# Performance work log

Measured on AMD Instinct MI355X. Metric: run time of the kernel, lower is better.

Reference implementation:

```python
import jax, jax.numpy as jnp
import numpy as np

# Synthetic taxonomy matching BuildDictionaries/Build_H_Matrix structure
N_O, N_F, N_G, N_S = 25, 150, 1200, 4800
PIQUETS = [0, N_O, N_O + N_F, N_O + N_F + N_G, N_O + N_F + N_G + N_S]  # [0,25,175,1375,6175]
C_TOTAL = PIQUETS[-1]
WEIGHTS = [0.25, 0.25, 0.15, 0.1]
E = float(np.e)
BATCH = 4096


def _build_H():
    H = np.zeros((C_TOTAL, C_TOTAL), dtype=np.float32)
    fam = np.arange(N_F)
    H[fam % N_O, PIQUETS[1] + fam] = 1.0              # order -> family
    gen = np.arange(N_G)
    H[PIQUETS[1] + gen % N_F, PIQUETS[2] + gen] = 1.0  # family -> genus
    sp = np.arange(N_S)
    H[PIQUETS[2] + sp % N_G, PIQUETS[3] + sp] = 1.0    # genus -> species
    return H


def setup_inputs() -> dict:
    key = jax.random.key(0)
    k1, k2 = jax.random.split(key)
    H_np = _build_H()
    # parent[j] = i such that H[i, j] == 1 (same as the get_grandparents row scan)
    parent_np = np.argmax(H_np, axis=0).astype(np.int64)
    y_pred = jax.random.normal(k1, (BATCH, C_TOTAL), dtype=jnp.float32)
    y_true = jax.random.randint(k2, (BATCH,), 0, N_S, dtype=jnp.int64)
    return {
        "y_pred": y_pred,
        "y_true": y_true,
        "H": jnp.asarray(H_np),
        "parent": jnp.asarray(parent_np),
    }


def _ce(logits, labels):
    # nn.CrossEntropyLoss with mean reduction
    logp = jax.nn.log_softmax(logits, axis=-1)
    return -jnp.mean(jnp.take_along_axis(logp, labels[:, None], axis=1))


def reference(y_pred, y_true, H, parent):
    nb_levels = 4
    # Per-level logit slices: y_pred[:, piquets[k]:piquets[k+1]]
    lp = [y_pred[:, PIQUETS[k]:PIQUETS[k + 1]] for k in range(nb_levels)]

    # Ancestor chain (vectorized get_grandparents): global ids per level
    g3 = y_true + PIQUETS[3]           # global species id (y_true += piquets[-2])
    g2 = parent[g3]                    # genus
    g1 = parent[g2]                    # family
    g0 = parent[g1]                    # order
    lt = [g0 - PIQUETS[0], g1 - PIQUETS[1], g2 - PIQUETS[2], g3 - PIQUETS[3]]

    # Faithful quirk: argmax indices are LOCAL to each level's slice,
    # and H is indexed with those local indices (as in the original code).
    argm = [jnp.argmax(x, axis=-1) for x in lp]

    s = _ce(lp[0], lt[0])
    loss = jnp.zeros((), dtype=y_pred.dtype)
    for k in range(1, nb_levels):
        h = H[argm[k - 1], argm[k]]                      # [B] gather
        pen = jnp.sum(jnp.where(h == 0, E, 0.0))         # sum_i (H==0)*e
        s = (s + pen + _ce(lp[k], lt[k])) * WEIGHTS[k]   # running sum *= weights[k]
        loss = loss + s
    return loss
```

## Files before the change

kernel.cpp:

```cpp
#include <hip/hip_runtime.h>
#include <math.h>

#define C_TOTAL 6175
#define BATCH 4096
#define NLEV 4

__device__ inline void am_merge(float& m, int& idx, float m2, int i2) {
    const bool take = (m2 > m) || (m2 == m && i2 < idx);
    idx = take ? i2 : idx;
    m   = fmaxf(m, m2);
}

__device__ inline void upd(float x, int i, float& m, float& s, int& ii) {
    s += __expf(x);
    ii = (x > m) ? i : ii;
    m  = fmaxf(m, x);
}

__device__ inline void butterfly(float& s, float& m, int& idx) {
    #pragma unroll
    for (int off = 1; off < 64; off <<= 1) {
        const float mm = __shfl_xor(m, off);
        const int   im = __shfl_xor(idx, off);
        const float sm = __shfl_xor(s, off);
        s += sm;
        am_merge(m, idx, mm, im);
    }
}

template <int W>
__device__ inline void process_span(const float* __restrict__ p,
                                    int lane, float& S, float& M, int& I) {
    if constexpr (W <= 64) {
        const float x = p[lane];
        const bool  a = (lane < W);
        float s = a ? __expf(x) : 0.f;
        float m = a ? x : -INFINITY;
        int idx = a ? lane : 0x7fffffff;
        butterfly(s, m, idx);
        S = s; M = m; I = idx;
        return;
    }

    float ms = -INFINITY, ss = 0.f;
    int   is_ = 0x7fffffff;

    int pe = (int)((4u - ((((uintptr_t)p) >> 2) & 3u)) & 3u);
    if (lane < pe) {
        const float x = p[lane];
        ss = __expf(x); ms = x; is_ = lane;
    }
    const int rem  = W - pe;
    const int nvec = rem >> 2;
    const int tail = rem & 3;
    const float4* vp = reinterpret_cast<const float4*>(p + pe);

    float m0 = -INFINITY, m1 = -INFINITY, m2 = -INFINITY, m3 = -INFINITY;
    float s0 = 0.f, s1 = 0.f, s2 = 0.f, s3 = 0.f;
    int   i0 = 0x1fffffff, i1 = 0x1fffffff, i2 = 0x1fffffff, i3 = 0x1fffffff;

    int i = lane;
    if constexpr (W >= 1024) {
        for (; i + 192 < nvec; i += 256) {
            const float4 a = vp[i];
            const float4 b = vp[i + 64];
            const float4 c = vp[i + 128];
            const float4 d = vp[i + 192];
            upd(a.x, i,       m0, s0, i0); upd(a.y, i,       m1, s1, i1);
            upd(a.z, i,       m2, s2, i2); upd(a.w, i,       m3, s3, i3);
            upd(b.x, i + 64,  m0, s0, i0); upd(b.y, i + 64,  m1, s1, i1);
            upd(b.z, i + 64,  m2, s2, i2); upd(b.w, i + 64,  m3, s3, i3);
            upd(c.x, i + 128, m0, s0, i0); upd(c.y, i + 128, m1, s1, i1);
            upd(c.z, i + 128, m2, s2, i2); upd(c.w, i + 128, m3, s3, i3);
            upd(d.x, i + 192, m0, s0, i0); upd(d.y, i + 192, m1, s1, i1);
            upd(d.z, i + 192, m2, s2, i2); upd(d.w, i + 192, m3, s3, i3);
        }
        for (; i + 64 < nvec; i += 128) {
            const float4 a = vp[i];
            const float4 b = vp[i + 64];
            upd(a.x, i, m0, s0, i0); upd(a.y, i, m1, s1, i1);
            upd(a.z, i, m2, s2, i2); upd(a.w, i, m3, s3, i3);
            upd(b.x, i + 64, m0, s0, i0); upd(b.y, i + 64, m1, s1, i1);
            upd(b.z, i + 64, m2, s2, i2); upd(b.w, i + 64, m3, s3, i3);
        }
    }
    for (; i < nvec; i += 64) {
        const float4 a = vp[i];
        upd(a.x, i, m0, s0, i0); upd(a.y, i, m1, s1, i1);
        upd(a.z, i, m2, s2, i2); upd(a.w, i, m3, s3, i3);
    }
    if (lane < tail) {
        const int c = pe + 4 * nvec + lane;
        const float x = p[c];
        ss += __expf(x);
        const bool take = (x > ms) || (x == ms && c < is_);
        is_ = take ? c : is_;
        ms  = fmaxf(ms, x);
    }

    float m = ms; int idx = is_;
    float s = ss + ((s0 + s1) + (s2 + s3));
    am_merge(m, idx, m0, pe + 4 * i0 + 0);
    am_merge(m, idx, m1, pe + 4 * i1 + 1);
    am_merge(m, idx, m2, pe + 4 * i2 + 2);
    am_merge(m, idx, m3, pe + 4 * i3 + 3);

    butterfly(s, m, idx);
    S = s; M = m; I = idx;
}

#define DO_SPAN(k, Wk)                                                      \
    {                                                                       \
        float S, M;                                                         \
        int I;                                                              \
        process_span<Wk>(rp + piq[k], lane, S, M, I);                       \
        ce[k]   = __logf(S) - rp[piq[k] + lab[k]];                          \
        argm[k] = I;                                                        \
    }

__global__ __launch_bounds__(256, 4) void taxa_row_kernel(
    const float* __restrict__ y_pred,
    const int*   __restrict__ y_true,
    const float* __restrict__ H,
    const int*   __restrict__ parent,
    float*       __restrict__ ws)
{
    constexpr int piq[5] = {0, 25, 175, 1375, 6175};
    const int lane = threadIdx.x & 63;
    const int wid  = threadIdx.x >> 6;
    const int row  = blockIdx.x * 4 + wid;
    const float* rp = y_pred + (long long)row * C_TOTAL;

    const int g3 = y_true[row] + 1375;
    const int g2 = parent[g3];
    const int g1 = parent[g2];
    const int g0 = parent[g1];
    int lab[NLEV];
    lab[0] = g0;
    lab[1] = g1 - 25;
    lab[2] = g2 - 175;
    lab[3] = g3 - 1375;

    float ce[NLEV];
    int   argm[NLEV];

    const int start = (blockIdx.x + wid) & 3;
    switch (start) {
        case 0: DO_SPAN(0, 25) DO_SPAN(1, 150) DO_SPAN(2, 1200) DO_SPAN(3, 4800) break;
        case 1: DO_SPAN(1, 150) DO_SPAN(2, 1200) DO_SPAN(3, 4800) DO_SPAN(0, 25) break;
        case 2: DO_SPAN(2, 1200) DO_SPAN(3, 4800) DO_SPAN(0, 25) DO_SPAN(1, 150) break;
        default: DO_SPAN(3, 4800) DO_SPAN(0, 25) DO_SPAN(1, 150) DO_SPAN(2, 1200) break;
    }

    if (lane == 0) {
        float h[3];
        #pragma unroll
        for (int k = 1; k < NLEV; ++k) {
            const float hv = H[(long long)argm[k - 1] * C_TOTAL + argm[k]];
            h[k - 1] = (hv == 0.f) ? 1.f : 0.f;
        }
        const float invB = 1.0f / 4096.0f;
        const float E    = 2.7182818284590452f;
        ws[row] = 0.29125f * ((ce[0] + ce[1]) * invB + E * h[0])
                + 0.165f  * (ce[2] * invB + E * h[1])
                + 0.10f   * (ce[3] * invB + E * h[2]);
    }
}

__global__ __launch_bounds__(256) void taxa_final_kernel(
    const float* __restrict__ ws, float* __restrict__ out)
{
    const int t = threadIdx.x;
    const float4* v = reinterpret_cast<const float4*>(ws);
    float a = 0.f;
    #pragma unroll
    for (int j = 0; j < 4; ++j) {
        const float4 x = v[t + 256 * j];
        a += (x.x + x.y) + (x.z + x.w);
    }
    #pragma unroll
    for (int off = 1; off < 64; off <<= 1) a += __shfl_xor(a, off);
    __shared__ float sm[4];
    if ((t & 63) == 0) sm[t >> 6] = a;
    __syncthreads();
    if (t == 0) out[0] = (sm[0] + sm[1]) + (sm[2] + sm[3]);
}

extern "C" void kernel_launch(void* const* d_in, const int* in_sizes, int n_in,
                              void* d_out, int out_size, void* d_ws, size_t ws_size,
                              hipStream_t stream) {
    const float* y_pred = (const float*)d_in[0];
    const int*   y_true = (const int*)d_in[1];
    const float* H      = (const float*)d_in[2];
    const int*   parent = (const int*)d_in[3];
    float* ws  = (float*)d_ws;
    float* out = (float*)d_out;

    taxa_row_kernel<<<dim3(BATCH / 4), dim3(256), 0, stream>>>(y_pred, y_true, H, parent, ws);
    taxa_final_kernel<<<dim3(1), dim3(256), 0, stream>>>(ws, out);
}
```

Baseline: 25.25 us.

## Process two rows per wavefront with interleaved loads for more memory-level parallelism

```diff
diff --git a/kernel.cpp b/kernel.cpp
--- a/kernel.cpp
+++ b/kernel.cpp
@@ -4,6 +4,7 @@
 #define C_TOTAL 6175
 #define BATCH 4096
 #define NLEV 4
+#define IBIG 0x1fffffff
 
 __device__ inline void am_merge(float& m, int& idx, float m2, int i2) {
     const bool take = (m2 > m) || (m2 == m && i2 < idx);
@@ -29,96 +30,126 @@
 }
 
 template <int W>
-__device__ inline void process_span(const float* __restrict__ p,
-                                    int lane, float& S, float& M, int& I) {
+__device__ inline void span2(const float* __restrict__ pA,
+                             const float* __restrict__ pB, int lane,
+                             float& SA, float& MA, int& IA,
+                             float& SB, float& MB, int& IB) {
     if constexpr (W <= 64) {
-        const float x = p[lane];
-        const bool  a = (lane < W);
-        float s = a ? __expf(x) : 0.f;
-        float m = a ? x : -INFINITY;
-        int idx = a ? lane : 0x7fffffff;
-        butterfly(s, m, idx);
-        S = s; M = m; I = idx;
+        const float xA = pA[lane];
+        const float xB = pB[lane];
+        const bool  a  = (lane < W);
+        float sA = a ? __expf(xA) : 0.f;
+        float mA = a ? xA : -INFINITY;
+        int   iA = a ? lane : 0x7fffffff;
+        float sB = a ? __expf(xB) : 0.f;
+        float mB = a ? xB : -INFINITY;
+        int   iB = a ? lane : 0x7fffffff;
+        butterfly(sA, mA, iA);
+        butterfly(sB, mB, iB);
+        SA = sA; MA = mA; IA = iA;
+        SB = sB; MB = mB; IB = iB;
         return;
     }
 
-    float ms = -INFINITY, ss = 0.f;
-    int   is_ = 0x7fffffff;
-
-    int pe = (int)((4u - ((((uintptr_t)p) >> 2) & 3u)) & 3u);
-    if (lane < pe) {
-        const float x = p[lane];
-        ss = __expf(x); ms = x; is_ = lane;
-    }
-    const int rem  = W - pe;
-    const int nvec = rem >> 2;
-    const int tail = rem & 3;
-    const float4* vp = reinterpret_cast<const float4*>(p + pe);
-
-    float m0 = -INFINITY, m1 = -INFINITY, m2 = -INFINITY, m3 = -INFINITY;
-    float s0 = 0.f, s1 = 0.f, s2 = 0.f, s3 = 0.f;
-    int   i0 = 0x1fffffff, i1 = 0x1fffffff, i2 = 0x1fffffff, i3 = 0x1fffffff;
-
+    const int peA = (int)((4u - ((((uintptr_t)pA) >> 2) & 3u)) & 3u);
+    const int peB = (int)((4u - ((((uintptr_t)pB) >> 2) & 3u)) & 3u);
+
+    float msA = -INFINITY, ssA = 0.f; int isA = 0x7fffffff;
+    float msB = -INFINITY, ssB = 0.f; int isB = 0x7fffffff;
+    if (lane < peA) { const float x = pA[lane]; ssA = __expf(x); msA = x; isA = lane; }
+    if (lane < peB) { const float x = pB[lane]; ssB = __expf(x); msB = x; isB = lane; }
+
+    const int nvA = (W - peA) >> 2, tlA = (W - peA) & 3;
+    const int nvB = (W - peB) >> 2, tlB = (W - peB) & 3;
+    const float4* vA = reinterpret_cast<const float4*>(pA + peA);
+    const float4* vB = reinterpret_cast<const float4*>(pB + peB);
+
+    float mA0=-INFINITY,mA1=-INFINITY,mA2=-INFINITY,mA3=-INFINITY;
+    float sA0=0.f,sA1=0.f,sA2=0.f,sA3=0.f;
+    int   iA0=IBIG,iA1=IBIG,iA2=IBIG,iA3=IBIG;
+    float mB0=-INFINITY,mB1=-INFINITY,mB2=-INFINITY,mB3=-INFINITY;
+    float sB0=0.f,sB1=0.f,sB2=0.f,sB3=0.f;
+    int   iB0=IBIG,iB1=IBIG,iB2=IBIG,iB3=IBIG;
+
+    const int nmin = nvA < nvB ? nvA : nvB;
     int i = lane;
     if constexpr (W >= 1024) {
-        for (; i + 192 < nvec; i += 256) {
-            const float4 a = vp[i];
-            const float4 b = vp[i + 64];
-            const float4 c = vp[i + 128];
-            const float4 d = vp[i + 192];
-            upd(a.x, i,       m0, s0, i0); upd(a.y, i,       m1, s1, i1);
-            upd(a.z, i,       m2, s2, i2); upd(a.w, i,       m3, s3, i3);
-            upd(b.x, i + 64,  m0, s0, i0); upd(b.y, i + 64,  m1, s1, i1);
-            upd(b.z, i + 64,  m2, s2, i2); upd(b.w, i + 64,  m3, s3, i3);
-            upd(c.x, i + 128, m0, s0, i0); upd(c.y, i + 128, m1, s1, i1);
-            upd(c.z, i + 128, m2, s2, i2); upd(c.w, i + 128, m3, s3, i3);
-            upd(d.x, i + 192, m0, s0, i0); upd(d.y, i + 192, m1, s1, i1);
-            upd(d.z, i + 192, m2, s2, i2); upd(d.w, i + 192, m3, s3, i3);
+        for (; i + 64 < nmin; i += 128) {
+            const float4 a0 = vA[i];
+            const float4 b0 = vB[i];
+            const float4 a1 = vA[i + 64];
+            const float4 b1 = vB[i + 64];
+            upd(a0.x, i,      mA0, sA0, iA0); upd(a0.y, i,      mA1, sA1, iA1);
+            upd(a0.z, i,      mA2, sA2, iA2); upd(a0.w, i,      mA3, sA3, iA3);
+            upd(b0.x, i,      mB0, sB0, iB0); upd(b0.y, i,      mB1, sB1, iB1);
+            upd(b0.z, i,      mB2, sB2, iB2); upd(b0.w, i,      mB3, sB3, iB3);
+            upd(a1.x, i + 64, mA0, sA0, iA0); upd(a1.y, i + 64, mA1, sA1, iA1);
+            upd(a1.z, i + 64, mA2, sA2, iA2); upd(a1.w, i + 64, mA3, sA3, iA3);
+            upd(b1.x, i + 64, mB0, sB0, iB0); upd(b1.y, i + 64, mB1, sB1, iB1);
+            upd(b1.z, i + 64, mB2, sB2, iB2); upd(b1.w, i + 64, mB3, sB3, iB3);
         }
-        for (; i + 64 < nvec; i += 128) {
-            const float4 a = vp[i];
-            const float4 b = vp[i + 64];
-            upd(a.x, i, m0, s0, i0); upd(a.y, i, m1, s1, i1);
-            upd(a.z, i, m2, s2, i2); upd(a.w, i, m3, s3, i3);
-            upd(b.x, i + 64, m0, s0, i0); upd(b.y, i + 64, m1, s1, i1);
-            upd(b.z, i + 64, m2, s2, i2); upd(b.w, i + 64, m3, s3, i3);
-        }
-    }
-    for (; i < nvec; i += 64) {
-        const float4 a = vp[i];
-        upd(a.x, i, m0, s0, i0); upd(a.y, i, m1, s1, i1);
-        upd(a.z, i, m2, s2, i2); upd(a.w, i, m3, s3, i3);
-    }
-    if (lane < tail) {
-        const int c = pe + 4 * nvec + lane;
-        const float x = p[c];
-        ss += __expf(x);
-        const bool take = (x > ms) || (x == ms && c < is_);
-        is_ = take ? c : is_;
-        ms  = fmaxf(ms, x);
-    }
-
-    float m = ms; int idx = is_;
-    float s = ss + ((s0 + s1) + (s2 + s3));
-    am_merge(m, idx, m0, pe + 4 * i0 + 0);
-    am_merge(m, idx, m1, pe + 4 * i1 + 1);
-    am_merge(m, idx, m2, pe + 4 * i2 + 2);
-    am_merge(m, idx, m3, pe + 4 * i3 + 3);
-
-    butterfly(s, m, idx);
-    S = s; M = m; I = idx;
-}
-
-#define DO_SPAN(k, Wk)                                                      \
+    }
+    int j = i;
+    for (; i < nvA; i += 64) {
+        const float4 a = vA[i];
+        upd(a.x, i, mA0, sA0, iA0); upd(a.y, i, mA1, sA1, iA1);
+        upd(a.z, i, mA2, sA2, iA2); upd(a.w, i, mA3, sA3, iA3);
+    }
+    for (; j < nvB; j += 64) {
+        const float4 b = vB[j];
+        upd(b.x, j, mB0, sB0, iB0); upd(b.y, j, mB1, sB1, iB1);
+        upd(b.z, j, mB2, sB2, iB2); upd(b.w, j, mB3, sB3, iB3);
+    }
+    if (lane < tlA) {
+        const int c = peA + 4 * nvA + lane;
+        const float x = pA[c];
+        ssA += __expf(x);
+        const bool take = (x > msA) || (x == msA && c < isA);
+        isA = take ? c : isA;
+        msA = fmaxf(msA, x);
+    }
+    if (lane < tlB) {
+        const int c = peB + 4 * nvB + lane;
+        const float x = pB[c];
+        ssB += __expf(x);
+        const bool take = (x > msB) || (x == msB && c < isB);
+        isB = take ? c : isB;
+        msB = fmaxf(msB, x);
+    }
+
+    {
+        float m = msA; int idx = isA;
+        float s = ssA + ((sA0 + sA1) + (sA2 + sA3));
+        am_merge(m, idx, mA0, peA + 4 * iA0 + 0);
+        am_merge(m, idx, mA1, peA + 4 * iA1 + 1);
+        am_merge(m, idx, mA2, peA + 4 * iA2 + 2);
+        am_merge(m, idx, mA3, peA + 4 * iA3 + 3);
+        butterfly(s, m, idx);
+        SA = s; MA = m; IA = idx;
+    }
+    {
+        float m = msB; int idx = isB;
+        float s = ssB + ((sB0 + sB1) + (sB2 + sB3));
+        am_merge(m, idx, mB0, peB + 4 * iB0 + 0);
+        am_merge(m, idx, mB1, peB + 4 * iB1 + 1);
+        am_merge(m, idx, mB2, peB + 4 * iB2 + 2);
+        am_merge(m, idx, mB3, peB + 4 * iB3 + 3);
+        butterfly(s, m, idx);
+        SB = s; MB = m; IB = idx;
+    }
+}
+
+#define DO_SPAN2(k, Wk)                                                     \
     {                                                                       \
-        float S, M;                                                         \
-        int I;                                                              \
-        process_span<Wk>(rp + piq[k], lane, S, M, I);                       \
-        ce[k]   = __logf(S) - rp[piq[k] + lab[k]];                          \
-        argm[k] = I;                                                        \
-    }
-
-__global__ __launch_bounds__(256, 4) void taxa_row_kernel(
+        float SA, MA, SB, MB;                                               \
+        int IA, IB;                                                         \
+        span2<Wk>(rpA + piq[k], rpB + piq[k], lane, SA, MA, IA, SB, MB, IB);\
+        ceA[k] = __logf(SA) - rpA[piq[k] + labA[k]];                        \
+        ceB[k] = __logf(SB) - rpB[piq[k] + labB[k]];                        \
+        argA[k] = IA; argB[k] = IB;                                         \
+    }
+
+__global__ __launch_bounds__(256, 2) void taxa_row_kernel(
     const float* __restrict__ y_pred,
     const int*   __restrict__ y_true,
     const float* __restrict__ H,
@@ -128,42 +159,50 @@
     constexpr int piq[5] = {0, 25, 175, 1375, 6175};
     const int lane = threadIdx.x & 63;
     const int wid  = threadIdx.x >> 6;
-    const int row  = blockIdx.x * 4 + wid;
-    const float* rp = y_pred + (long long)row * C_TOTAL;
-
-    const int g3 = y_true[row] + 1375;
-    const int g2 = parent[g3];
-    const int g1 = parent[g2];
-    const int g0 = parent[g1];
-    int lab[NLEV];
-    lab[0] = g0;
-    lab[1] = g1 - 25;
-    lab[2] = g2 - 175;
-    lab[3] = g3 - 1375;
-
-    float ce[NLEV];
-    int   argm[NLEV];
+    const int rA   = (blockIdx.x * 4 + wid) * 2;
+    const int rB   = rA + 1;
+    const float* rpA = y_pred + (long long)rA * C_TOTAL;
+    const float* rpB = y_pred + (long long)rB * C_TOTAL;
+
+    const int g3A = y_true[rA] + 1375;
+    const int g2A = parent[g3A];
+    const int g1A = parent[g2A];
+    const int g0A = parent[g1A];
+    const int g3B = y_true[rB] + 1375;
+    const int g2B = parent[g3B];
+    const int g1B = parent[g2B];
+    const int g0B = parent[g1B];
+    int labA[NLEV] = {g0A, g1A - 25, g2A - 175, g3A - 1375};
+    int labB[NLEV] = {g0B, g1B - 25, g2B - 175, g3B - 1375};
+
+    float ceA[NLEV], ceB[NLEV];
+    int   argA[NLEV], argB[NLEV];
 
     const int start = (blockIdx.x + wid) & 3;
     switch (start) {
-        case 0: DO_SPAN(0, 25) DO_SPAN(1, 150) DO_SPAN(2, 1200) DO_SPAN(3, 4800) break;
-        case 1: DO_SPAN(1, 150) DO_SPAN(2, 1200) DO_SPAN(3, 4800) DO_SPAN(0, 25) break;
-        case 2: DO_SPAN(2, 1200) DO_SPAN(3, 4800) DO_SPAN(0, 25) DO_SPAN(1, 150) break;
-        default: DO_SPAN(3, 4800) DO_SPAN(0, 25) DO_SPAN(1, 150) DO_SPAN(2, 1200) break;
+        case 0: DO_SPAN2(0, 25) DO_SPAN2(1, 150) DO_SPAN2(2, 1200) DO_SPAN2(3, 4800) break;
+        case 1: DO_SPAN2(1, 150) DO_SPAN2(2, 1200) DO_SPAN2(3, 4800) DO_SPAN2(0, 25) break;
+        case 2: DO_SPAN2(2, 1200) DO_SPAN2(3, 4800) DO_SPAN2(0, 25) DO_SPAN2(1, 150) break;
+        default: DO_SPAN2(3, 4800) DO_SPAN2(0, 25) DO_SPAN2(1, 150) DO_SPAN2(2, 1200) break;
     }
 
     if (lane == 0) {
-        float h[3];
+        const float invB = 1.0f / 4096.0f;
+        const float E    = 2.7182818284590452f;
+        float hA[3], hB[3];
         #pragma unroll
         for (int k = 1; k < NLEV; ++k) {
-            const float hv = H[(long long)argm[k - 1] * C_TOTAL + argm[k]];
-            h[k - 1] = (hv == 0.f) ? 1.f : 0.f;
+            const float ha = H[(long long)argA[k - 1] * C_TOTAL + argA[k]];
+            const float hb = H[(long long)argB[k - 1] * C_TOTAL + argB[k]];
+            hA[k - 1] = (ha == 0.f) ? 1.f : 0.f;
+            hB[k - 1] = (hb == 0.f) ? 1.f : 0.f;
         }
-        const float invB = 1.0f / 4096.0f;
-        const float E    = 2.7182818284590452f;
-        ws[row] = 0.29125f * ((ce[0] + ce[1]) * invB + E * h[0])
-                + 0.165f  * (ce[2] * invB + E * h[1])
-                + 0.10f   * (ce[3] * invB + E * h[2]);
+        ws[rA] = 0.29125f * ((ceA[0] + ceA[1]) * invB + E * hA[0])
+               + 0.165f  * (ceA[2] * invB + E * hA[1])
+               + 0.10f   * (ceA[3] * invB + E * hA[2]);
+        ws[rB] = 0.29125f * ((ceB[0] + ceB[1]) * invB + E * hB[0])
+               + 0.165f  * (ceB[2] * invB + E * hB[1])
+               + 0.10f   * (ceB[3] * invB + E * hB[2]);
     }
 }
 
@@ -196,6 +235,6 @@
     float* ws  = (float*)d_ws;
     float* out = (float*)d_out;
 
-    taxa_row_kernel<<<dim3(BATCH / 4), dim3(256), 0, stream>>>(y_pred, y_true, H, parent, ws);
+    taxa_row_kernel<<<dim3(BATCH / 8), dim3(256), 0, stream>>>(y_pred, y_true, H, parent, ws);
     taxa_final_kernel<<<dim3(1), dim3(256), 0, stream>>>(ws, out);
 }
```

Result: slower. 29.71 us (+17.7%).
